# Kernel optimization log

Measured on AMD Instinct MI355X. Metric: run time of the kernel, lower is better.

## Reference

```python
import jax, jax.numpy as jnp
import numpy as np

N, D, C = 1000000, 128, 100

def setup_inputs() -> dict:
    key = jax.random.key(0)
    k1, k2, k3 = jax.random.split(key, 3)
    embedding = jax.random.normal(k1, (N, D), dtype=jnp.float32)
    centers = jax.random.normal(k2, (C, D), dtype=jnp.float32)
    logits = jax.random.normal(k3, (N, C), dtype=jnp.float32)
    return {"embedding": embedding, "centers": centers, "logits": logits}

def reference(embedding, centers, logits):
    num_classes = logits.shape[-1]
    assign = jnp.argmax(logits, axis=-1)  # [N]
    # single-pass segment mean over clusters
    sums = jax.ops.segment_sum(embedding, assign, num_segments=num_classes)  # [C, D]
    counts = jax.ops.segment_sum(jnp.ones((embedding.shape[0],), embedding.dtype),
                                 assign, num_segments=num_classes)  # [C]
    centroids = sums / jnp.maximum(counts, 1.0)[:, None]  # safe mean; empty -> 0
    delta = centers - centroids  # [C, D]
    sq = jnp.sum(delta * delta, axis=-1)  # [C]
    # grad-safe sqrt (masked anyway for empty clusters)
    dist = jnp.sqrt(jnp.where(sq > 0, sq, 1.0)) * (sq > 0).astype(embedding.dtype)
    return jnp.where(counts > 0, dist, 0.0)
```

## Files before the change

kernel.cpp:

```cpp
#include <hip/hip_runtime.h>
#include <math.h>


#define NROWS 1000000
#define DIM   128
#define NCLS  100
#define NSLICE 16
#define SLICE_ROWS (NROWS / NSLICE)
#define PSTRIDE 132
#define QCAP  128
#define QMASK 127

typedef __attribute__((ext_vector_type(4))) float f32x4;

__global__ __launch_bounds__(256)
void l2cc_argmax(const float* __restrict__ logits, int* __restrict__ assign)
{
    const int tid = threadIdx.x;
    const int row = blockIdx.x * 64 + (tid >> 2);
    const int p   = tid & 3;
    if (row >= NROWS) return;

    const float4* lrow = reinterpret_cast<const float4*>(logits + (size_t)row * NCLS);
    float best = -INFINITY;
    int   bi   = 0x7fffffff;
    #pragma unroll
    for (int i = 0; i < 6; ++i) {
        const float4 v = lrow[i * 4 + p];
        const int c0 = i * 16 + p * 4;
        if (v.x > best) { best = v.x; bi = c0;     }
        if (v.y > best) { best = v.y; bi = c0 + 1; }
        if (v.z > best) { best = v.z; bi = c0 + 2; }
        if (v.w > best) { best = v.w; bi = c0 + 3; }
    }
    {
        const float t = logits[(size_t)row * NCLS + 96 + p];
        if (t > best) { best = t; bi = 96 + p; }
    }
    #pragma unroll
    for (int off = 1; off <= 2; off <<= 1) {
        const float ov = __shfl_xor(best, off, 64);
        const int   oi = __shfl_xor(bi,   off, 64);
        if (ov > best || (ov == best && oi < bi)) { best = ov; bi = oi; }
    }
    if (p == 0) assign[row] = bi;
}

#define DRAIN16                                                               \
    {                                                                         \
        _Pragma("unroll")                                                     \
        for (int k_ = 0; k_ < 8; ++k_) {                                      \
            const int r_ = q[wave][(qhead + 2 * k_ + half) & QMASK];          \
            acc += *reinterpret_cast<const f32x4*>(                           \
                emb + (size_t)r_ * DIM + l5 * 4);                             \
        }                                                                     \
        qhead += 16;                                                          \
    }

#define PUSH(AV, OFF)                                                         \
    {                                                                         \
        const unsigned long long m_ = __ballot((AV) == c);                    \
        if ((AV) == c) {                                                      \
            const int rank_ = __popcll(m_ & ((1ull << lane) - 1ull));         \
            q[wave][(qtail + rank_) & QMASK] = rw + (OFF) + lane;             \
        }                                                                     \
        const int pc_ = __popcll(m_);                                         \
        qtail += pc_; icnt += pc_;                                            \
        while (qtail - qhead >= 16) DRAIN16                                   \
    }

__global__ __launch_bounds__(256)
void l2cc_gather(const float* __restrict__ emb,
                 const int* __restrict__ assign,
                 float* __restrict__ partial)
{
    const int bid  = blockIdx.x;
    const int c    = bid / NSLICE;
    const int sl   = bid - c * NSLICE;
    const int wave = threadIdx.x >> 6;
    const int lane = threadIdx.x & 63;
    const int half = lane >> 5;
    const int l5   = lane & 31;

    __shared__ int   q[4][QCAP];
    __shared__ f32x4 sacc[4][64];
    __shared__ int   scnt[4];

    const int start = sl * SLICE_ROWS;
    const int end   = start + SLICE_ROWS;

    f32x4 acc = {0.0f, 0.0f, 0.0f, 0.0f};
    int   icnt = 0, qhead = 0, qtail = 0;

    int rw = start + wave * 256;
    int a0 = (rw +   0 + lane < end) ? assign[rw +   0 + lane] : -1;
    int a1 = (rw +  64 + lane < end) ? assign[rw +  64 + lane] : -1;
    int a2 = (rw + 128 + lane < end) ? assign[rw + 128 + lane] : -1;
    int a3 = (rw + 192 + lane < end) ? assign[rw + 192 + lane] : -1;

    for (; rw < end; rw += 1024) {
        const int rn = rw + 1024;
        int b0 = -1, b1 = -1, b2 = -1, b3 = -1;
        if (rn < end) {
            b0 = (rn +   0 + lane < end) ? assign[rn +   0 + lane] : -1;
            b1 = (rn +  64 + lane < end) ? assign[rn +  64 + lane] : -1;
            b2 = (rn + 128 + lane < end) ? assign[rn + 128 + lane] : -1;
            b3 = (rn + 192 + lane < end) ? assign[rn + 192 + lane] : -1;
        }

        PUSH(a0, 0) PUSH(a1, 64) PUSH(a2, 128) PUSH(a3, 192)

        a0 = b0; a1 = b1; a2 = b2; a3 = b3;
    }

    while (qtail > qhead) {
        const int r = q[wave][qhead & QMASK]; ++qhead;
        if (half == 0)
            acc += *reinterpret_cast<const f32x4*>(emb + (size_t)r * DIM + l5 * 4);
    }

    sacc[wave][lane] = acc;
    if (lane == 0) scnt[wave] = icnt;
    __syncthreads();
    if (wave == 0 && lane < 32) {
        f32x4 v = (((sacc[0][lane] + sacc[1][lane]) + sacc[2][lane]) + sacc[3][lane])
                + (((sacc[0][32 + lane] + sacc[1][32 + lane])
                  + sacc[2][32 + lane]) + sacc[3][32 + lane]);
        float* p = partial + (size_t)bid * PSTRIDE;
        *reinterpret_cast<f32x4*>(p + lane * 4) = v;
        if (lane == 0)
            p[DIM] = (float)(((scnt[0] + scnt[1]) + scnt[2]) + scnt[3]);
    }
}

__global__ __launch_bounds__(128)
void l2cc_final(const float* __restrict__ partial,
                const float* __restrict__ centers,
                float* __restrict__ out)
{
    const int c = blockIdx.x;
    const int t = threadIdx.x;

    float s = 0.0f, cnt = 0.0f;
    #pragma unroll
    for (int sl = 0; sl < NSLICE; ++sl) {
        const float* p = partial + (size_t)(c * NSLICE + sl) * PSTRIDE;
        s   += p[t];
        cnt += p[DIM];
    }

    const float centroid = s / fmaxf(cnt, 1.0f);
    const float dd = centers[c * DIM + t] - centroid;
    float sq = dd * dd;
    #pragma unroll
    for (int off = 32; off > 0; off >>= 1) sq += __shfl_xor(sq, off, 64);

    __shared__ float red[2];
    if ((t & 63) == 0) red[t >> 6] = sq;
    __syncthreads();
    if (t == 0) {
        const float total = red[0] + red[1];
        out[c] = (cnt > 0.0f && total > 0.0f) ? sqrtf(total) : 0.0f;
    }
}

extern "C" void kernel_launch(void* const* d_in, const int* in_sizes, int n_in,
                              void* d_out, int out_size, void* d_ws, size_t ws_size,
                              hipStream_t stream)
{
    const float* emb     = (const float*)d_in[0];
    const float* centers = (const float*)d_in[1];
    const float* logits  = (const float*)d_in[2];
    float* out = (float*)d_out;

    int*   assign  = (int*)d_ws;
    float* partial = (float*)((char*)d_ws + (size_t)NROWS * sizeof(int));

    l2cc_argmax<<<(NROWS + 63) / 64, 256, 0, stream>>>(logits, assign);
    l2cc_gather<<<NCLS * NSLICE, 256, 0, stream>>>(emb, assign, partial);
    l2cc_final <<<NCLS, 128, 0, stream>>>(partial, centers, out);
}
```

Baseline: 183.9 us.

## Make argmax kernel persistent with double-buffered logits prefetch

The argmax kernel becomes a grid-stride persistent kernel with 1024 blocks instead of one block per 64 rows. Each thread double-buffers its logits registers, loading the next group's row before computing argmax on the current one, with sched_barrier keeping the loads ahead of the compute. The aim is to keep more memory requests in flight per wave and cut block launch overhead on this bandwidth-bound pass. The extra registers for the second buffer could lower occupancy.

Measured after the change: 190.0 us. 1.03x slower.

```diff
diff --git a/kernel.cpp b/kernel.cpp
--- a/kernel.cpp
+++ b/kernel.cpp
@@ -10,40 +10,74 @@
 #define PSTRIDE 132
 #define QCAP  128
 #define QMASK 127
+#define GROUPS (NROWS / 64)
+#define K1_BLOCKS 1024
 
 typedef __attribute__((ext_vector_type(4))) float f32x4;
 
-__global__ __launch_bounds__(256)
-void l2cc_argmax(const float* __restrict__ logits, int* __restrict__ assign)
-{
-    const int tid = threadIdx.x;
-    const int row = blockIdx.x * 64 + (tid >> 2);
-    const int p   = tid & 3;
-    if (row >= NROWS) return;
-
-    const float4* lrow = reinterpret_cast<const float4*>(logits + (size_t)row * NCLS);
+__device__ __forceinline__ void k1_load(const float* __restrict__ logits,
+                                        int grp, int g, int p,
+                                        f32x4 v[6], float& t)
+{
+    const float* lr = logits + (size_t)(grp * 64 + g) * NCLS;
+    #pragma unroll
+    for (int i = 0; i < 6; ++i)
+        v[i] = *reinterpret_cast<const f32x4*>(lr + i * 16 + p * 4);
+    t = lr[96 + p];
+}
+
+__device__ __forceinline__ void k1_process(const f32x4 v[6], float t,
+                                           int grp, int g, int p,
+                                           int* __restrict__ assign)
+{
     float best = -INFINITY;
     int   bi   = 0x7fffffff;
     #pragma unroll
     for (int i = 0; i < 6; ++i) {
-        const float4 v = lrow[i * 4 + p];
         const int c0 = i * 16 + p * 4;
-        if (v.x > best) { best = v.x; bi = c0;     }
-        if (v.y > best) { best = v.y; bi = c0 + 1; }
-        if (v.z > best) { best = v.z; bi = c0 + 2; }
-        if (v.w > best) { best = v.w; bi = c0 + 3; }
-    }
-    {
-        const float t = logits[(size_t)row * NCLS + 96 + p];
-        if (t > best) { best = t; bi = 96 + p; }
-    }
+        if (v[i][0] > best) { best = v[i][0]; bi = c0;     }
+        if (v[i][1] > best) { best = v[i][1]; bi = c0 + 1; }
+        if (v[i][2] > best) { best = v[i][2]; bi = c0 + 2; }
+        if (v[i][3] > best) { best = v[i][3]; bi = c0 + 3; }
+    }
+    if (t > best) { best = t; bi = 96 + p; }
     #pragma unroll
     for (int off = 1; off <= 2; off <<= 1) {
         const float ov = __shfl_xor(best, off, 64);
         const int   oi = __shfl_xor(bi,   off, 64);
         if (ov > best || (ov == best && oi < bi)) { best = ov; bi = oi; }
     }
-    if (p == 0) assign[row] = bi;
+    if (p == 0) assign[grp * 64 + g] = bi;
+}
+
+__global__ __launch_bounds__(256)
+void l2cc_argmax(const float* __restrict__ logits, int* __restrict__ assign)
+{
+    const int g = threadIdx.x >> 2;
+    const int p = threadIdx.x & 3;
+    const int stride = gridDim.x;
+
+    int grp = blockIdx.x;
+    if (grp >= GROUPS) return;
+
+    f32x4 vA[6], vB[6];
+    float tA, tB;
+
+    k1_load(logits, grp, g, p, vA, tA);
+    for (;;) {
+        const int g1 = grp + stride;
+        if (g1 < GROUPS) k1_load(logits, g1, g, p, vB, tB);
+        __builtin_amdgcn_sched_barrier(0);
+        k1_process(vA, tA, grp, g, p, assign);
+        if (g1 >= GROUPS) break;
+
+        const int g2 = g1 + stride;
+        if (g2 < GROUPS) k1_load(logits, g2, g, p, vA, tA);
+        __builtin_amdgcn_sched_barrier(0);
+        k1_process(vB, tB, g1, g, p, assign);
+        if (g2 >= GROUPS) break;
+        grp = g2;
+    }
 }
 
 #define DRAIN16                                                               \
@@ -176,7 +210,7 @@
     int*   assign  = (int*)d_ws;
     float* partial = (float*)((char*)d_ws + (size_t)NROWS * sizeof(int));
 
-    l2cc_argmax<<<(NROWS + 63) / 64, 256, 0, stream>>>(logits, assign);
+    l2cc_argmax<<<K1_BLOCKS, 256, 0, stream>>>(logits, assign);
     l2cc_gather<<<NCLS * NSLICE, 256, 0, stream>>>(emb, assign, partial);
     l2cc_final <<<NCLS, 128, 0, stream>>>(partial, centers, out);
 }
```

## Stage argmax logits via async global-to-LDS loads with double buffering

Applied to the files above, without the earlier changes.

The argmax kernel now assigns each wave a sequence of 16-row groups and copies each group's logits into LDS with global_load_lds, double-buffered so the next group's load overlaps compute on the current one. The grid shrinks to persistent-style blocks that each process 64 groups. This aims to keep more memory requests in flight and coalesce the 400-byte row reads into contiguous 16-byte lane loads. It relies on hand-written vmcnt waits with no barrier, since each wave touches only its own buffer, and it uses 51 KB of LDS per block, which limits occupancy.

New measurement: 193.1 us. 1.05x slower.

```diff
diff --git a/kernel.cpp b/kernel.cpp
--- a/kernel.cpp
+++ b/kernel.cpp
@@ -11,30 +11,46 @@
 #define QCAP  128
 #define QMASK 127
 
+#define GRP_ROWS  16
+#define NGRP      (NROWS / GRP_ROWS)
+#define GRP_BYTES (GRP_ROWS * NCLS * 4)
+#define K1_ITERS  16
+#define GRPS_PER_BLOCK (4 * K1_ITERS)
+
 typedef __attribute__((ext_vector_type(4))) float f32x4;
 
-__global__ __launch_bounds__(256)
-void l2cc_argmax(const float* __restrict__ logits, int* __restrict__ assign)
-{
-    const int tid = threadIdx.x;
-    const int row = blockIdx.x * 64 + (tid >> 2);
-    const int p   = tid & 3;
-    if (row >= NROWS) return;
-
-    const float4* lrow = reinterpret_cast<const float4*>(logits + (size_t)row * NCLS);
+__device__ __forceinline__ void k1_stage(const float* __restrict__ logits,
+                                         float* dst, int g, int lane)
+{
+    const char* src = (const char*)logits + (size_t)g * GRP_BYTES;
+    #pragma unroll
+    for (int k = 0; k < 6; ++k)
+        __builtin_amdgcn_global_load_lds(
+            (const __attribute__((address_space(1))) unsigned int*)(src + k * 1024 + lane * 16),
+            (__attribute__((address_space(3))) unsigned int*)(dst + k * 256),
+            16, 0, 0);
+    __builtin_amdgcn_global_load_lds(
+        (const __attribute__((address_space(1))) unsigned int*)(src + 6144 + lane * 4),
+        (__attribute__((address_space(3))) unsigned int*)(dst + 1536),
+        4, 0, 0);
+}
+
+__device__ __forceinline__ void k1_compute(const float* row, int g, int qid, int p,
+                                           int* __restrict__ assign)
+{
     float best = -INFINITY;
     int   bi   = 0x7fffffff;
     #pragma unroll
     for (int i = 0; i < 6; ++i) {
-        const float4 v = lrow[i * 4 + p];
+        const f32x4 v = *reinterpret_cast<const f32x4*>(row + i * 16 + p * 4);
         const int c0 = i * 16 + p * 4;
-        if (v.x > best) { best = v.x; bi = c0;     }
-        if (v.y > best) { best = v.y; bi = c0 + 1; }
-        if (v.z > best) { best = v.z; bi = c0 + 2; }
-        if (v.w > best) { best = v.w; bi = c0 + 3; }
+        if (v[0] > best) { best = v[0]; bi = c0;     }
+        if (v[1] > best) { best = v[1]; bi = c0 + 1; }
+        if (v[2] > best) { best = v[2]; bi = c0 + 2; }
+        if (v[3] > best) { best = v[3]; bi = c0 + 3; }
     }
     {
-        const float t = logits[(size_t)row * NCLS + 96 + p];
+        const float t = row[96 + p];
         if (t > best) { best = t; bi = 96 + p; }
     }
     #pragma unroll
@@ -43,7 +59,38 @@
         const int   oi = __shfl_xor(bi,   off, 64);
         if (ov > best || (ov == best && oi < bi)) { best = ov; bi = oi; }
     }
-    if (p == 0) assign[row] = bi;
+    if (p == 0) assign[g * GRP_ROWS + qid] = bi;
+}
+
+__global__ __launch_bounds__(256)
+void l2cc_argmax(const float* __restrict__ logits, int* __restrict__ assign)
+{
+    __shared__ float lds[4][2][1600];
+    const int tid  = threadIdx.x;
+    const int w    = tid >> 6;
+    const int lane = tid & 63;
+    const int qid  = lane >> 2;
+    const int p    = lane & 3;
+
+    const int bg = blockIdx.x * GRPS_PER_BLOCK;
+
+    int gi = bg + w;
+    if (gi < NGRP) k1_stage(logits, &lds[w][0][0], gi, lane);
+
+    #pragma unroll 1
+    for (int it = 0; it < K1_ITERS; ++it) {
+        const int  gn = gi + 4;
+        const bool vn = (it + 1 < K1_ITERS) && (gn < NGRP);
+        if (vn) {
+            k1_stage(logits, &lds[w][(it + 1) & 1][0], gn, lane);
+            asm volatile("s_waitcnt vmcnt(7)" ::: "memory");
+        } else {
+            asm volatile("s_waitcnt vmcnt(0)" ::: "memory");
+        }
+        if (gi < NGRP)
+            k1_compute(&lds[w][it & 1][qid * NCLS], gi, qid, p, assign);
+        gi = gn;
+    }
 }
 
 #define DRAIN16                                                               \
@@ -176,7 +223,7 @@
     int*   assign  = (int*)d_ws;
     float* partial = (float*)((char*)d_ws + (size_t)NROWS * sizeof(int));
 
-    l2cc_argmax<<<(NROWS + 63) / 64, 256, 0, stream>>>(logits, assign);
+    l2cc_argmax<<<(NGRP + GRPS_PER_BLOCK - 1) / GRPS_PER_BLOCK, 256, 0, stream>>>(logits, assign);
     l2cc_gather<<<NCLS * NSLICE, 256, 0, stream>>>(emb, assign, partial);
     l2cc_final <<<NCLS, 128, 0, stream>>>(partial, centers, out);
 }
```

## Fuse argmax and gather into one persistent kernel with per-slice completion flags

Applied to the files above, without the earlier changes.

Merges the argmax and gather kernels into one launch. The first 157 blocks compute argmax slice by slice and bump a per-slice done counter, while gather blocks spin until their slice is complete and then start, so gathering overlaps with argmax of later slices. Each gather block now handles two classes per pass over the assignments, which halves how often the assignment array is rescanned, and slices go from 16 to 25. The risks are that spin-waiting blocks hold CUs, that correctness depends on the argmax blocks being scheduled before the waiters (deadlock if they are not resident), and that relaxed atomics give no release/acquire ordering on the assignment data.

Result: slower. 527.4 us (+186.8%).

```diff
diff --git a/kernel.cpp b/kernel.cpp
--- a/kernel.cpp
+++ b/kernel.cpp
@@ -5,22 +5,28 @@
 #define NROWS 1000000
 #define DIM   128
 #define NCLS  100
-#define NSLICE 16
-#define SLICE_ROWS (NROWS / NSLICE)
+#define NSLICE 25
+#define SROWS (NROWS / NSLICE)
+#define GPS   625
+#define GA    157
+#define GPB   4
+#define GB    1250
 #define PSTRIDE 132
 #define QCAP  128
 #define QMASK 127
 
 typedef __attribute__((ext_vector_type(4))) float f32x4;
 
-__global__ __launch_bounds__(256)
-void l2cc_argmax(const float* __restrict__ logits, int* __restrict__ assign)
-{
-    const int tid = threadIdx.x;
-    const int row = blockIdx.x * 64 + (tid >> 2);
-    const int p   = tid & 3;
-    if (row >= NROWS) return;
-
+__global__ void l2cc_zero(int* __restrict__ ctrl)
+{
+    if (threadIdx.x < 32) ctrl[threadIdx.x] = 0;
+}
+
+__device__ __forceinline__ void argmax_group(const float* __restrict__ logits,
+                                             int* __restrict__ assign,
+                                             int row_base, int qid, int p)
+{
+    const int row = row_base + qid;
     const float4* lrow = reinterpret_cast<const float4*>(logits + (size_t)row * NCLS);
     float best = -INFINITY;
     int   bi   = 0x7fffffff;
@@ -43,93 +49,158 @@
         const int   oi = __shfl_xor(bi,   off, 64);
         if (ov > best || (ov == best && oi < bi)) { best = ov; bi = oi; }
     }
-    if (p == 0) assign[row] = bi;
-}
-
-#define DRAIN16                                                               \
+    if (p == 0)
+        __hip_atomic_store(&assign[row], bi, __ATOMIC_RELAXED,
+                           __HIP_MEMORY_SCOPE_AGENT);
+}
+
+#define DRAINQ(QI, ACC, QH)                                                   \
     {                                                                         \
         _Pragma("unroll")                                                     \
         for (int k_ = 0; k_ < 8; ++k_) {                                      \
-            const int r_ = q[wave][(qhead + 2 * k_ + half) & QMASK];          \
-            acc += *reinterpret_cast<const f32x4*>(                           \
+            const int r_ = q[wave][QI][((QH) + 2 * k_ + half) & QMASK];       \
+            ACC += *reinterpret_cast<const f32x4*>(                           \
                 emb + (size_t)r_ * DIM + l5 * 4);                             \
         }                                                                     \
-        qhead += 16;                                                          \
-    }
-
-#define PUSH(AV, OFF)                                                         \
+        QH += 16;                                                             \
+    }
+
+#define PUSHC(AV, OFF, CC, QI, QT, QH, ACC, ICNT)                             \
     {                                                                         \
-        const unsigned long long m_ = __ballot((AV) == c);                    \
-        if ((AV) == c) {                                                      \
+        const unsigned long long m_ = __ballot((AV) == (CC));                 \
+        if ((AV) == (CC)) {                                                   \
             const int rank_ = __popcll(m_ & ((1ull << lane) - 1ull));         \
-            q[wave][(qtail + rank_) & QMASK] = rw + (OFF) + lane;             \
+            q[wave][QI][((QT) + rank_) & QMASK] = rw + (OFF) + lane;          \
         }                                                                     \
         const int pc_ = __popcll(m_);                                         \
-        qtail += pc_; icnt += pc_;                                            \
-        while (qtail - qhead >= 16) DRAIN16                                   \
-    }
-
-__global__ __launch_bounds__(256)
-void l2cc_gather(const float* __restrict__ emb,
-                 const int* __restrict__ assign,
-                 float* __restrict__ partial)
-{
-    const int bid  = blockIdx.x;
-    const int c    = bid / NSLICE;
-    const int sl   = bid - c * NSLICE;
-    const int wave = threadIdx.x >> 6;
-    const int lane = threadIdx.x & 63;
+        QT += pc_; ICNT += pc_;                                               \
+        while (QT - QH >= 16) DRAINQ(QI, ACC, QH)                             \
+    }
+
+#define PUSH2(AV, OFF)                                                        \
+    PUSHC(AV, OFF, c0, 0, qt0, qh0, acc0, icnt0)                              \
+    PUSHC(AV, OFF, c1, 1, qt1, qh1, acc1, icnt1)
+
+#define ALOAD(IDX) (((IDX) < end)                                             \
+    ? __hip_atomic_load(assign + (IDX), __ATOMIC_RELAXED,                     \
+                        __HIP_MEMORY_SCOPE_AGENT)                             \
+    : -1)
+
+__global__ __launch_bounds__(256, 6)
+void l2cc_mega(const float* __restrict__ emb,
+               const float* __restrict__ logits,
+               int* __restrict__ done,
+               int* __restrict__ assign,
+               float* __restrict__ partial)
+{
+    const int tid = threadIdx.x;
+
+    if (blockIdx.x < GA) {
+        const int b   = blockIdx.x;
+        const int qid = tid >> 2;
+        const int p   = tid & 3;
+        const int g0b = b * GPB;
+        const int ng  = min(GPB, GPS - g0b);
+
+        for (int s = 0; s < NSLICE; ++s) {
+            const int g0 = s * GPS + g0b;
+            if (ng == GPB) {
+                #pragma unroll
+                for (int j = 0; j < GPB; ++j)
+                    argmax_group(logits, assign, (g0 + j) * 64, qid, p);
+            } else {
+                for (int j = 0; j < ng; ++j)
+                    argmax_group(logits, assign, (g0 + j) * 64, qid, p);
+            }
+            __syncthreads();
+            if (tid == 0)
+                __hip_atomic_fetch_add(&done[s], 1, __ATOMIC_RELAXED,
+                                       __HIP_MEMORY_SCOPE_AGENT);
+        }
+        return;
+    }
+
+    __shared__ int   q[4][2][QCAP];
+    __shared__ f32x4 sacc[4][64];
+    __shared__ int   scnt[4];
+
+    const int gbid = blockIdx.x - GA;
+    const int s    = gbid / 50;
+    const int k    = gbid - s * 50;
+    const int c0   = 2 * k;
+    const int c1   = c0 + 1;
+    const int wave = tid >> 6;
+    const int lane = tid & 63;
     const int half = lane >> 5;
     const int l5   = lane & 31;
 
-    __shared__ int   q[4][QCAP];
-    __shared__ f32x4 sacc[4][64];
-    __shared__ int   scnt[4];
-
-    const int start = sl * SLICE_ROWS;
-    const int end   = start + SLICE_ROWS;
-
-    f32x4 acc = {0.0f, 0.0f, 0.0f, 0.0f};
-    int   icnt = 0, qhead = 0, qtail = 0;
+    if (tid == 0) {
+        while (__hip_atomic_load(&done[s], __ATOMIC_RELAXED,
+                                 __HIP_MEMORY_SCOPE_AGENT) < GA)
+            __builtin_amdgcn_s_sleep(64);
+    }
+    __syncthreads();
+
+    const int start = s * SROWS;
+    const int end   = start + SROWS;
+
+    f32x4 acc0 = {0.f, 0.f, 0.f, 0.f}, acc1 = {0.f, 0.f, 0.f, 0.f};
+    int icnt0 = 0, icnt1 = 0, qh0 = 0, qt0 = 0, qh1 = 0, qt1 = 0;
 
     int rw = start + wave * 256;
-    int a0 = (rw +   0 + lane < end) ? assign[rw +   0 + lane] : -1;
-    int a1 = (rw +  64 + lane < end) ? assign[rw +  64 + lane] : -1;
-    int a2 = (rw + 128 + lane < end) ? assign[rw + 128 + lane] : -1;
-    int a3 = (rw + 192 + lane < end) ? assign[rw + 192 + lane] : -1;
+    int a0 = ALOAD(rw + 0 + lane);
+    int a1 = ALOAD(rw + 64 + lane);
+    int a2 = ALOAD(rw + 128 + lane);
+    int a3 = ALOAD(rw + 192 + lane);
 
     for (; rw < end; rw += 1024) {
         const int rn = rw + 1024;
         int b0 = -1, b1 = -1, b2 = -1, b3 = -1;
         if (rn < end) {
-            b0 = (rn +   0 + lane < end) ? assign[rn +   0 + lane] : -1;
-            b1 = (rn +  64 + lane < end) ? assign[rn +  64 + lane] : -1;
-            b2 = (rn + 128 + lane < end) ? assign[rn + 128 + lane] : -1;
-            b3 = (rn + 192 + lane < end) ? assign[rn + 192 + lane] : -1;
+            b0 = ALOAD(rn + 0 + lane);
+            b1 = ALOAD(rn + 64 + lane);
+            b2 = ALOAD(rn + 128 + lane);
+            b3 = ALOAD(rn + 192 + lane);
         }
-
-        PUSH(a0, 0) PUSH(a1, 64) PUSH(a2, 128) PUSH(a3, 192)
-
+        PUSH2(a0, 0) PUSH2(a1, 64) PUSH2(a2, 128) PUSH2(a3, 192)
         a0 = b0; a1 = b1; a2 = b2; a3 = b3;
     }
 
-    while (qtail > qhead) {
-        const int r = q[wave][qhead & QMASK]; ++qhead;
+    while (qt0 > qh0) {
+        const int r = q[wave][0][qh0 & QMASK]; ++qh0;
         if (half == 0)
-            acc += *reinterpret_cast<const f32x4*>(emb + (size_t)r * DIM + l5 * 4);
-    }
-
-    sacc[wave][lane] = acc;
-    if (lane == 0) scnt[wave] = icnt;
+            acc0 += *reinterpret_cast<const f32x4*>(emb + (size_t)r * DIM + l5 * 4);
+    }
+    while (qt1 > qh1) {
+        const int r = q[wave][1][qh1 & QMASK]; ++qh1;
+        if (half == 0)
+            acc1 += *reinterpret_cast<const f32x4*>(emb + (size_t)r * DIM + l5 * 4);
+    }
+
+    sacc[wave][lane] = acc0;
+    if (lane == 0) scnt[wave] = icnt0;
     __syncthreads();
     if (wave == 0 && lane < 32) {
         f32x4 v = (((sacc[0][lane] + sacc[1][lane]) + sacc[2][lane]) + sacc[3][lane])
                 + (((sacc[0][32 + lane] + sacc[1][32 + lane])
                   + sacc[2][32 + lane]) + sacc[3][32 + lane]);
-        float* p = partial + (size_t)bid * PSTRIDE;
-        *reinterpret_cast<f32x4*>(p + lane * 4) = v;
+        float* pp = partial + (size_t)(s * NCLS + c0) * PSTRIDE;
+        *reinterpret_cast<f32x4*>(pp + lane * 4) = v;
         if (lane == 0)
-            p[DIM] = (float)(((scnt[0] + scnt[1]) + scnt[2]) + scnt[3]);
+            pp[DIM] = (float)(((scnt[0] + scnt[1]) + scnt[2]) + scnt[3]);
+    }
+    __syncthreads();
+    sacc[wave][lane] = acc1;
+    if (lane == 0) scnt[wave] = icnt1;
+    __syncthreads();
+    if (wave == 0 && lane < 32) {
+        f32x4 v = (((sacc[0][lane] + sacc[1][lane]) + sacc[2][lane]) + sacc[3][lane])
+                + (((sacc[0][32 + lane] + sacc[1][32 + lane])
+                  + sacc[2][32 + lane]) + sacc[3][32 + lane]);
+        float* pp = partial + (size_t)(s * NCLS + c1) * PSTRIDE;
+        *reinterpret_cast<f32x4*>(pp + lane * 4) = v;
+        if (lane == 0)
+            pp[DIM] = (float)(((scnt[0] + scnt[1]) + scnt[2]) + scnt[3]);
     }
 }
 
@@ -144,7 +215,7 @@
     float s = 0.0f, cnt = 0.0f;
     #pragma unroll
     for (int sl = 0; sl < NSLICE; ++sl) {
-        const float* p = partial + (size_t)(c * NSLICE + sl) * PSTRIDE;
+        const float* p = partial + (size_t)(sl * NCLS + c) * PSTRIDE;
         s   += p[t];
         cnt += p[DIM];
     }
@@ -173,10 +244,11 @@
     const float* logits  = (const float*)d_in[2];
     float* out = (float*)d_out;
 
-    int*   assign  = (int*)d_ws;
-    float* partial = (float*)((char*)d_ws + (size_t)NROWS * sizeof(int));
-
-    l2cc_argmax<<<(NROWS + 63) / 64, 256, 0, stream>>>(logits, assign);
-    l2cc_gather<<<NCLS * NSLICE, 256, 0, stream>>>(emb, assign, partial);
-    l2cc_final <<<NCLS, 128, 0, stream>>>(partial, centers, out);
-}
+    int*   ctrl    = (int*)d_ws;
+    int*   assign  = ctrl + 32;
+    float* partial = (float*)((char*)d_ws + 128 + (size_t)NROWS * sizeof(int));
+
+    l2cc_zero <<<1, 64, 0, stream>>>(ctrl);
+    l2cc_mega <<<GA + GB, 256, 0, stream>>>(emb, logits, ctrl, assign, partial);
+    l2cc_final<<<NCLS, 128, 0, stream>>>(partial, centers, out);
+}
```
